# Kernel optimization log

Hardware: AMD Instinct MI355X
Metric: run time of the kernel (lower is better)

Reference implementation:

```python
import jax, jax.numpy as jnp
import numpy as np

CHANNELS = 256
N_HEADS = 8
WS = 8
HEAD_DIM = CHANNELS // N_HEADS
SCALE = HEAD_DIM ** -0.5
EPS = 1e-5


def setup_inputs() -> dict:
    key = jax.random.key(0)
    ks = jax.random.split(key, 7)
    C = CHANNELS
    B, T, H, W = 2, 4, 64, 64
    x = jax.random.normal(ks[0], (B * T, C, H, W), dtype=jnp.float32)
    s = 1.0 / np.sqrt(C)
    w_qkv = jax.random.uniform(ks[1], (3 * C, C), jnp.float32, -s, s)
    b_qkv = jax.random.uniform(ks[2], (3 * C,), jnp.float32, -s, s)
    w_proj = jax.random.uniform(ks[3], (C, C), jnp.float32, -s, s)
    b_proj = jax.random.uniform(ks[4], (C,), jnp.float32, -s, s)
    gamma = jnp.ones((C,), jnp.float32)
    beta = jnp.zeros((C,), jnp.float32)
    return {"x": x, "w_qkv": w_qkv, "b_qkv": b_qkv, "w_proj": w_proj,
            "b_proj": b_proj, "gamma": gamma, "beta": beta, "T": T}


def _forward(x, w_qkv, b_qkv, w_proj, b_proj, gamma, beta, T):
    BT, C, H, W = x.shape
    B = BT // T
    ws = WS
    pH = (ws - H % ws) % ws
    pW = (ws - W % ws) % ws
    if pH > 0 or pW > 0:
        x_p = jnp.pad(x, ((0, 0), (0, 0), (0, pH), (0, pW)))
    else:
        x_p = x
    Hp, Wp = H + pH, W + pW
    nH, nW = Hp // ws, Wp // ws
    # partition: (B,T,C,nH,ws,nW,ws) -> (B,nH,nW,T,ws,ws,C) -> (B*nH*nW, T*ws*ws, C)
    xw = x_p.reshape(B, T, C, nH, ws, nW, ws)
    xw = jnp.transpose(xw, (0, 3, 5, 1, 4, 6, 2))
    L = T * ws * ws
    xw = xw.reshape(B * nH * nW, L, C)
    # LayerNorm over channels
    mu = jnp.mean(xw, axis=-1, keepdims=True)
    var = jnp.mean(jnp.square(xw - mu), axis=-1, keepdims=True)
    xn = (xw - mu) * jax.lax.rsqrt(var + EPS) * gamma + beta
    # QKV projection
    qkv = xn @ w_qkv.T + b_qkv  # (NW, L, 3C)
    qkv = qkv.reshape(xw.shape[0], L, 3, N_HEADS, HEAD_DIM)
    q, k, v = qkv[:, :, 0], qkv[:, :, 1], qkv[:, :, 2]  # (NW, L, h, d)
    scores = jnp.einsum('nlhd,nmhd->nhlm', q, k) * SCALE
    attn = jax.nn.softmax(scores, axis=-1)
    out = jnp.einsum('nhlm,nmhd->nlhd', attn, v).reshape(xw.shape[0], L, C)
    out = out @ w_proj.T + b_proj
    out = xw + out
    # unpartition
    out = out.reshape(B, nH, nW, T, ws, ws, C)
    out = jnp.transpose(out, (0, 3, 6, 1, 4, 2, 5)).reshape(B * T, C, Hp, Wp)
    if pH > 0 or pW > 0:
        out = out[:, :, :H, :W]
    return out


def reference(x, w_qkv, b_qkv, w_proj, b_proj, gamma, beta, T):
    return _forward(x, w_qkv, b_qkv, w_proj, b_proj, gamma, beta, T)
```

## Files before the change

kernel.cpp:

```cpp
#include <hip/hip_runtime.h>
#include <hip/hip_bf16.h>

typedef __hip_bfloat16 bf16;
typedef __attribute__((ext_vector_type(8))) short short8;
typedef __attribute__((ext_vector_type(4))) short sh4;
typedef __attribute__((ext_vector_type(4))) float f32x4;

#define SCALE_F 0.17677669529663687f
#define LOG2E_F 1.4426950408889634f
#define EPS_F 1e-5f
#define NW_CHUNK 32
#define ROWS_CHUNK (NW_CHUNK * 256)

#define OW_QKV  0
#define OW_PROJ 196608
#define OB_QKV  262144
#define OB_PROJ 262912
#define NWB     263168

__device__ __forceinline__ float b2f(bf16 v) { return __bfloat162float(v); }
__device__ __forceinline__ bf16 f2b(float v) { return __float2bfloat16(v); }
__device__ __forceinline__ short f2bs(float v) { bf16 h = f2b(v); return *(short*)&h; }
__device__ __forceinline__ float bs2f(short s) { bf16 h = *(bf16*)&s; return __bfloat162float(h); }

__device__ __forceinline__ float ldin(const void* p, size_t i, int mode) {
  if (mode) return ((const float*)p)[i];
  return b2f(((const bf16*)p)[i]);
}
__device__ __forceinline__ void stout(void* p, size_t i, int mode, float v) {
  if (mode) ((float*)p)[i] = v;
  else      ((bf16*)p)[i] = f2b(v);
}
__device__ __forceinline__ float4 ldin4(const void* p, size_t i, int mode) {
  if (mode) return *(const float4*)((const float*)p + i);
  const sh4 s = *(const sh4*)((const short*)p + i);
  return make_float4(bs2f(s[0]), bs2f(s[1]), bs2f(s[2]), bs2f(s[3]));
}
__device__ __forceinline__ void stout4(void* p, size_t i, int mode, float4 v) {
  if (mode) { *(float4*)((float*)p + i) = v; }
  else {
    sh4 s; s[0] = f2bs(v.x); s[1] = f2bs(v.y); s[2] = f2bs(v.z); s[3] = f2bs(v.w);
    *(sh4*)((short*)p + i) = s;
  }
}

__device__ __forceinline__ void gld16(void* lds, const void* g) {
  __builtin_amdgcn_global_load_lds(
      (const __attribute__((address_space(1))) unsigned int*)g,
      (__attribute__((address_space(3))) unsigned int*)lds, 16, 0, 0);
}

__global__ __launch_bounds__(256) void k_probe(const float* __restrict__ xf,
                                               int* __restrict__ flag) {
  __shared__ int cnt;
  if (threadIdx.x == 0) cnt = 0;
  __syncthreads();
  int bad = 0;
  for (int i = threadIdx.x; i < 1024; i += 256) {
    const float v = xf[i];
    if (!(fabsf(v) < 1e20f)) bad++;
  }
  atomicAdd(&cnt, bad);
  __syncthreads();
  if (threadIdx.x == 0) flag[0] = (cnt < 8) ? 1 : 0;
}

__global__ __launch_bounds__(256) void k_prep(const void* __restrict__ w1,
                                              const void* __restrict__ w2,
                                              const void* __restrict__ b1,
                                              const void* __restrict__ b2,
                                              short* __restrict__ wbuf,
                                              const int* __restrict__ flag) {
  const int mode = flag[0];
  const int i = blockIdx.x * 256 + threadIdx.x;
  float v;
  if (i < OW_PROJ)      v = ldin(w1, i, mode);
  else if (i < OB_QKV)  v = ldin(w2, i - OW_PROJ, mode);
  else if (i < OB_PROJ) v = ldin(b1, i - OB_QKV, mode);
  else if (i < NWB)     v = ldin(b2, i - OB_PROJ, mode);
  else return;
  wbuf[i] = f2bs(v);
}

__global__ __launch_bounds__(256) void k_ln(const void* __restrict__ x,
                                            const void* __restrict__ gamma,
                                            const void* __restrict__ beta,
                                            bf16* __restrict__ xn,
                                            const int* __restrict__ flag) {
  const int mode = flag[0];
  const int bt = blockIdx.x >> 6;
  const int h  = blockIdx.x & 63;
  const int tid = threadIdx.x;
  const int cl = tid >> 4;
  const int wi = tid & 15;

  __shared__ short sX[256][68];
  __shared__ float sred[16][65];
  __shared__ float sqred[16][65];
  __shared__ float smu[64], srs[64];

  const size_t gbase = (size_t)bt * 1048576 + (size_t)h * 64 + wi * 4;
  float s4[4] = {0.f, 0.f, 0.f, 0.f}, q4[4] = {0.f, 0.f, 0.f, 0.f};
  for (int c0 = 0; c0 < 256; c0 += 16) {
    const int c = c0 + cl;
    const float4 v = ldin4(x, gbase + (size_t)c * 4096, mode);
    s4[0] += v.x; q4[0] += v.x * v.x;
    s4[1] += v.y; q4[1] += v.y * v.y;
    s4[2] += v.z; q4[2] += v.z * v.z;
    s4[3] += v.w; q4[3] += v.w * v.w;
    sh4 b;
    b[0] = f2bs(v.x); b[1] = f2bs(v.y); b[2] = f2bs(v.z); b[3] = f2bs(v.w);
    *(sh4*)&sX[c][wi * 4] = b;
  }
#pragma unroll
  for (int k = 0; k < 4; ++k) {
    sred[cl][wi * 4 + k] = s4[k];
    sqred[cl][wi * 4 + k] = q4[k];
  }
  __syncthreads();
  if (tid < 64) {
    float a = 0.f, q = 0.f;
#pragma unroll
    for (int g = 0; g < 16; ++g) { a += sred[g][tid]; q += sqred[g][tid]; }
    const float mu = a * (1.0f / 256.0f);
    const float var = fmaxf(q * (1.0f / 256.0f) - mu * mu, 0.0f);
    smu[tid] = mu; srs[tid] = rsqrtf(var + EPS_F);
  }
  __syncthreads();

  const int c = tid;
  const float g = ldin(gamma, c, mode), be = ldin(beta, c, mode);
  const size_t rb =
      ((size_t)(((bt >> 2) * 64 + (h >> 3) * 8) * 256 + (bt & 3) * 64 + (h & 7) * 8)) * 256 + c;
  for (int iw = 0; iw < 8; ++iw) {
#pragma unroll
    for (int s = 0; s < 8; ++s) {
      const int w = iw * 8 + s;
      const float v = bs2f(sX[c][w]);
      xn[rb + (size_t)iw * 65536 + s * 256] = f2b((v - smu[w]) * srs[w] * g + be);
    }
  }
}

__global__ __launch_bounds__(256) void k_qkv(const bf16* __restrict__ A,
                                             const short* __restrict__ wb,
                                             bf16* __restrict__ out,
                                             int row_base) {
  __shared__ short smem[2 * 128 * 72];
  short* sA = smem;
  short* sB = smem + 128 * 64;
  const int row0 = blockIdx.x * 128;
  const int col0 = blockIdx.y * 128;
  const int tid = threadIdx.x;
  const int wid = tid >> 6, lane = tid & 63;
  const int wy = wid >> 1, wx = wid & 1;
  const int l15 = lane & 15, quad = lane >> 4;
  const short* Ab = (const short*)A;

  const int lr = lane >> 3;
  const int swc = (lane & 7) ^ lr;

  f32x4 acc[4][4];
#pragma unroll
  for (int i = 0; i < 4; ++i)
#pragma unroll
    for (int j = 0; j < 4; ++j) acc[i][j] = (f32x4){0.f, 0.f, 0.f, 0.f};

  for (int k0 = 0; k0 < 256; k0 += 64) {
    if (k0) __syncthreads();
#pragma unroll
    for (int it = 0; it < 4; ++it) {
      const int rbase = wid * 32 + it * 8;
      gld16(sA + rbase * 64,
            Ab + (size_t)(row_base + row0 + rbase + lr) * 256 + k0 + swc * 8);
      gld16(sB + rbase * 64,
            wb + (size_t)(col0 + rbase + lr) * 256 + k0 + swc * 8);
    }
    asm volatile("s_waitcnt vmcnt(0)" ::: "memory");
    __syncthreads();
#pragma unroll
    for (int kk = 0; kk < 64; kk += 32) {
      const int ck = kk >> 3;
      short8 af[4], bfv[4];
#pragma unroll
      for (int i = 0; i < 4; ++i) {
        const int ar = wy * 64 + i * 16 + l15;
        af[i] = *(const short8*)(sA + ar * 64 + (((quad + ck) ^ (ar & 7)) * 8));
      }
#pragma unroll
      for (int j = 0; j < 4; ++j) {
        const int br = wx * 64 + j * 16 + l15;
        bfv[j] = *(const short8*)(sB + br * 64 + (((quad + ck) ^ (br & 7)) * 8));
      }
#pragma unroll
      for (int i = 0; i < 4; ++i)
#pragma unroll
        for (int j = 0; j < 4; ++j)
          acc[i][j] = __builtin_amdgcn_mfma_f32_16x16x32_bf16(af[i], bfv[j], acc[i][j], 0, 0, 0);
    }
  }

  __syncthreads();
  short* slab = smem + wid * (64 * 72);
#pragma unroll
  for (int j = 0; j < 4; ++j) {
    const int col = col0 + wx * 64 + j * 16 + l15;
    const float bj = bs2f(wb[OB_QKV + col]);
#pragma unroll
    for (int i = 0; i < 4; ++i)
#pragma unroll
      for (int r = 0; r < 4; ++r)
        slab[(i * 16 + quad * 4 + r) * 72 + j * 16 + l15] = f2bs(acc[i][j][r] + bj);
  }
  asm volatile("s_waitcnt lgkmcnt(0)" ::: "memory");
  {
    const int srow = lane >> 3;
    const int scol = (lane & 7) * 8;
    short* og = (short*)out;
#pragma unroll
    for (int it = 0; it < 8; ++it) {
      const int rloc = it * 8 + srow;
      short8 v = *(const short8*)&slab[rloc * 72 + scol];
      *(short8*)&og[(size_t)(row0 + wy * 64 + rloc) * 768 + col0 + wx * 64 + scol] = v;
    }
  }
}

__global__ __launch_bounds__(256) void k_attn(const bf16* __restrict__ qkv,
                                              bf16* __restrict__ aout,
                                              int n_base, int nw_mask, int nw_shift) {
  const int n_loc = blockIdx.x & nw_mask, hh = blockIdx.x >> nw_shift;
  const int n_glob = n_base + n_loc;
  __shared__ short sK[256][32];
  __shared__ short sVt[32][256];
  __shared__ short sP[4][16][64];
  const int tid = threadIdx.x;
  const int wid = tid >> 6, lane = tid & 63;
  const int l15 = lane & 15, quad = lane >> 4;
  const short* qg = (const short*)qkv;
  const size_t base = (size_t)n_loc * 256 * 768 + hh * 32;

#pragma unroll
  for (int it = 0; it < 4; ++it) {
    const int rbase = wid * 64 + it * 16;
    gld16(&sK[rbase][0],
          qg + base + (size_t)(rbase + (lane >> 2)) * 768 + 256 + (lane & 3) * 8);
  }
  for (int c = tid; c < 1024; c += 256) {
    const int m = c >> 2, d0 = (c & 3) * 8;
    short8 vv = *(const short8*)(qg + base + (size_t)m * 768 + 512 + d0);
#pragma unroll
    for (int j = 0; j < 8; ++j)
      sVt[d0 + j][(((m >> 3) ^ j) << 3) | (m & 7)] = vv[j];
  }
  asm volatile("s_waitcnt vmcnt(0)" ::: "memory");
  __syncthreads();

  const int R0 = wid * 64;
  const float esc = SCALE_F * LOG2E_F;

  for (int lt = 0; lt < 4; ++lt) {
    const int lrow = R0 + lt * 16;
    const short8 qf = *(const short8*)(qg + base + (size_t)(lrow + l15) * 768 + quad * 8);

    f32x4 sacc[16];
    __builtin_amdgcn_s_setprio(1);
#pragma unroll
    for (int t = 0; t < 16; ++t) {
      sacc[t] = (f32x4){0.f, 0.f, 0.f, 0.f};
      const short8 kf = *(const short8*)&sK[t * 16 + l15][quad * 8];
      sacc[t] = __builtin_amdgcn_mfma_f32_16x16x32_bf16(qf, kf, sacc[t], 0, 0, 0);
    }
    __builtin_amdgcn_s_setprio(0);

    float sum[4] = {0.f, 0.f, 0.f, 0.f};
#pragma unroll
    for (int t = 0; t < 16; ++t)
#pragma unroll
      for (int r = 0; r < 4; ++r) {
        const float p = exp2f(sacc[t][r] * esc);
        sacc[t][r] = p;
        sum[r] += p;
      }
#pragma unroll
    for (int m = 1; m < 16; m <<= 1)
#pragma unroll
      for (int r = 0; r < 4; ++r) sum[r] += __shfl_xor(sum[r], m, 64);
    float inv[4];
#pragma unroll
    for (int r = 0; r < 4; ++r) inv[r] = 1.0f / sum[r];

    f32x4 oacc[2] = {(f32x4){0.f, 0.f, 0.f, 0.f}, (f32x4){0.f, 0.f, 0.f, 0.f}};
#pragma unroll
    for (int ph = 0; ph < 4; ++ph) {
#pragma unroll
      for (int t = 0; t < 4; ++t) {
        const int tt = ph * 4 + t;
        const int chnk = t * 2 + (l15 >> 3);
#pragma unroll
        for (int r = 0; r < 4; ++r) {
          const int row = quad * 4 + r;
          sP[wid][row][((chnk ^ (row & 7)) << 3) | (l15 & 7)] = f2bs(sacc[tt][r]);
        }
      }
      asm volatile("s_waitcnt lgkmcnt(0)" ::: "memory");
      __builtin_amdgcn_s_setprio(1);
#pragma unroll
      for (int kk = 0; kk < 2; ++kk) {
        const int pch = (kk * 4 + quad) ^ (l15 & 7);
        const short8 pf = *(const short8*)&sP[wid][l15][pch * 8];
#pragma unroll
        for (int dt = 0; dt < 2; ++dt) {
          const int vrow = dt * 16 + l15;
          const int cch = ph * 8 + kk * 4 + quad;
          const short8 vf = *(const short8*)&sVt[vrow][((cch ^ (vrow & 7)) * 8)];
          oacc[dt] = __builtin_amdgcn_mfma_f32_16x16x32_bf16(pf, vf, oacc[dt], 0, 0, 0);
        }
      }
      __builtin_amdgcn_s_setprio(0);
      asm volatile("s_waitcnt lgkmcnt(0)" ::: "memory");
    }

#pragma unroll
    for (int dt = 0; dt < 2; ++dt) {
      const int chnk = dt * 2 + (l15 >> 3);
#pragma unroll
      for (int r = 0; r < 4; ++r) {
        const int row = quad * 4 + r;
        sP[wid][row][((chnk ^ (row & 7)) << 3) | (l15 & 7)] = f2bs(oacc[dt][r] * inv[r]);
      }
    }
    asm volatile("s_waitcnt lgkmcnt(0)" ::: "memory");
    {
      const int rloc = lane >> 2;
      const int pch = (lane & 3) ^ (rloc & 7);
      short8 v = *(const short8*)&sP[wid][rloc][pch * 8];
      short* og = (short*)aout;
      *(short8*)&og[((size_t)n_glob * 256 + lrow + rloc) * 256 + hh * 32 + (lane & 3) * 8] = v;
    }
    asm volatile("s_waitcnt lgkmcnt(0)" ::: "memory");
  }
}

__global__ __launch_bounds__(256) void k_proj_g(const bf16* __restrict__ A,
                                                const short* __restrict__ wb,
                                                bf16* __restrict__ out) {
  __shared__ short smem[2 * 128 * 72];
  short* sA = smem;
  short* sB = smem + 128 * 64;
  const int row0 = blockIdx.x * 128;
  const int col0 = blockIdx.y * 128;
  const int tid = threadIdx.x;
  const int wid = tid >> 6, lane = tid & 63;
  const int wy = wid >> 1, wx = wid & 1;
  const int l15 = lane & 15, quad = lane >> 4;
  const short* Ab = (const short*)A;

  const int lr = lane >> 3;
  const int swc = (lane & 7) ^ lr;

  f32x4 acc[4][4];
#pragma unroll
  for (int i = 0; i < 4; ++i)
#pragma unroll
    for (int j = 0; j < 4; ++j) acc[i][j] = (f32x4){0.f, 0.f, 0.f, 0.f};

  for (int k0 = 0; k0 < 256; k0 += 64) {
    if (k0) __syncthreads();
#pragma unroll
    for (int it = 0; it < 4; ++it) {
      const int rbase = wid * 32 + it * 8;
      gld16(sA + rbase * 64,
            Ab + (size_t)(row0 + rbase + lr) * 256 + k0 + swc * 8);
      gld16(sB + rbase * 64,
            wb + OW_PROJ + (size_t)(col0 + rbase + lr) * 256 + k0 + swc * 8);
    }
    asm volatile("s_waitcnt vmcnt(0)" ::: "memory");
    __syncthreads();
#pragma unroll
    for (int kk = 0; kk < 64; kk += 32) {
      const int ck = kk >> 3;
      short8 af[4], bfv[4];
#pragma unroll
      for (int i = 0; i < 4; ++i) {
        const int ar = wy * 64 + i * 16 + l15;
        af[i] = *(const short8*)(sA + ar * 64 + (((quad + ck) ^ (ar & 7)) * 8));
      }
#pragma unroll
      for (int j = 0; j < 4; ++j) {
        const int br = wx * 64 + j * 16 + l15;
        bfv[j] = *(const short8*)(sB + br * 64 + (((quad + ck) ^ (br & 7)) * 8));
      }
#pragma unroll
      for (int i = 0; i < 4; ++i)
#pragma unroll
        for (int j = 0; j < 4; ++j)
          acc[i][j] = __builtin_amdgcn_mfma_f32_16x16x32_bf16(af[i], bfv[j], acc[i][j], 0, 0, 0);
    }
  }

  __syncthreads();
  short* slab = smem + wid * (64 * 72);
#pragma unroll
  for (int j = 0; j < 4; ++j) {
    const int col = col0 + wx * 64 + j * 16 + l15;
    const float bj = bs2f(wb[OB_PROJ + col]);
#pragma unroll
    for (int i = 0; i < 4; ++i)
#pragma unroll
      for (int r = 0; r < 4; ++r)
        slab[(i * 16 + quad * 4 + r) * 72 + j * 16 + l15] = f2bs(acc[i][j][r] + bj);
  }
  asm volatile("s_waitcnt lgkmcnt(0)" ::: "memory");
  {
    const int srow = lane >> 3;
    const int scol = (lane & 7) * 8;
    short* og = (short*)out;
#pragma unroll
    for (int it = 0; it < 8; ++it) {
      const int rloc = it * 8 + srow;
      short8 v = *(const short8*)&slab[rloc * 72 + scol];
      *(short8*)&og[(size_t)(row0 + wy * 64 + rloc) * 256 + col0 + wx * 64 + scol] = v;
    }
  }
}

__global__ __launch_bounds__(256) void k_add(const bf16* __restrict__ tmp,
                                             const void* __restrict__ x,
                                             void* __restrict__ out,
                                             const int* __restrict__ flag) {
  const int mode = flag[0];
  const int bt = blockIdx.x >> 6;
  const int h  = blockIdx.x & 63;
  const int tid = threadIdx.x;

  __shared__ short sT2[256][68];

  const int n_b = (bt >> 2) * 64 + (h >> 3) * 8;
  const int l0  = (bt & 3) * 64 + (h & 7) * 8;
  const short* tg = (const short*)tmp;

#pragma unroll
  for (int i = 0; i < 8; ++i) {
    const int id = i * 256 + tid;
    const int w = id >> 5, c8 = (id & 31) * 8;
    const int row = (n_b + (w >> 3)) * 256 + l0 + (w & 7);
    const short8 v = *(const short8*)(tg + (size_t)row * 256 + c8);
    const int wg = ((w >> 2) ^ ((id & 31) & 15)) * 4 + (w & 3);
#pragma unroll
    for (int j = 0; j < 8; ++j) sT2[c8 + j][wg] = v[j];
  }
  __syncthreads();

  const int cl = tid >> 4;
  const int wi = tid & 15;
  const size_t gb = (size_t)bt * 1048576 + (size_t)h * 64 + wi * 4;
  for (int c0 = 0; c0 < 256; c0 += 16) {
    const int c = c0 + cl;
    const int k15 = (c >> 3) & 15;
    const sh4 pv = *(const sh4*)&sT2[c][((wi ^ k15) & 15) * 4];
    const size_t gaddr = gb + (size_t)c * 4096;
    const float4 xv = ldin4(x, gaddr, mode);
    float4 o;
    o.x = xv.x + bs2f(pv[0]);
    o.y = xv.y + bs2f(pv[1]);
    o.z = xv.z + bs2f(pv[2]);
    o.w = xv.w + bs2f(pv[3]);
    stout4(out, gaddr, mode, o);
  }
}

__global__ __launch_bounds__(256) void k_proj(const bf16* __restrict__ A,
                                              const short* __restrict__ wb,
                                              const void* __restrict__ x,
                                              void* __restrict__ out,
                                              const int* __restrict__ flag) {
  const int mode = flag[0];
  __shared__ short smem[2 * 128 * 64];
  __shared__ float sT[4][16][17];
  short* sA = smem;
  short* sB = smem + 128 * 64;
  const int row0 = blockIdx.x * 128;
  const int col0 = blockIdx.y * 128;
  const int tid = threadIdx.x;
  const int wid = tid >> 6, lane = tid & 63;
  const int wy = wid >> 1, wx = wid & 1;
  const int l15 = lane & 15, quad = lane >> 4;
  const short* Ab = (const short*)A;

  const int lr = lane >> 3;
  const int swc = (lane & 7) ^ lr;

  f32x4 acc[4][4];
#pragma unroll
  for (int i = 0; i < 4; ++i)
#pragma unroll
    for (int j = 0; j < 4; ++j) acc[i][j] = (f32x4){0.f, 0.f, 0.f, 0.f};

  for (int k0 = 0; k0 < 256; k0 += 64) {
    if (k0) __syncthreads();
#pragma unroll
    for (int it = 0; it < 4; ++it) {
      const int rbase = wid * 32 + it * 8;
      gld16(sA + rbase * 64,
            Ab + (size_t)(row0 + rbase + lr) * 256 + k0 + swc * 8);
      gld16(sB + rbase * 64,
            wb + OW_PROJ + (size_t)(col0 + rbase + lr) * 256 + k0 + swc * 8);
    }
    asm volatile("s_waitcnt vmcnt(0)" ::: "memory");
    __syncthreads();
#pragma unroll
    for (int kk = 0; kk < 64; kk += 32) {
      const int ck = kk >> 3;
      short8 af[4], bfv[4];
#pragma unroll
      for (int i = 0; i < 4; ++i) {
        const int ar = wy * 64 + i * 16 + l15;
        af[i] = *(const short8*)(sA + ar * 64 + (((quad + ck) ^ (ar & 7)) * 8));
      }
#pragma unroll
      for (int j = 0; j < 4; ++j) {
        const int br = wx * 64 + j * 16 + l15;
        bfv[j] = *(const short8*)(sB + br * 64 + (((quad + ck) ^ (br & 7)) * 8));
      }
#pragma unroll
      for (int i = 0; i < 4; ++i)
#pragma unroll
        for (int j = 0; j < 4; ++j)
          acc[i][j] = __builtin_amdgcn_mfma_f32_16x16x32_bf16(af[i], bfv[j], acc[i][j], 0, 0, 0);
    }
  }

#pragma unroll
  for (int i = 0; i < 4; ++i) {
#pragma unroll
    for (int j = 0; j < 4; ++j) {
#pragma unroll
      for (int r = 0; r < 4; ++r)
        sT[wid][quad * 4 + r][l15] = acc[i][j][r];
      asm volatile("s_waitcnt lgkmcnt(0)" ::: "memory");
#pragma unroll
      for (int r2 = 0; r2 < 4; ++r2) {
        const float v = sT[wid][l15][quad * 4 + r2];
        const int row = row0 + wy * 64 + i * 16 + l15;
        const int c   = col0 + wx * 64 + j * 16 + quad * 4 + r2;
        const int n = row >> 8, l = row & 255;
        const int b = n >> 6, ih = (n >> 3) & 7, iw = n & 7;
        const int tt = l >> 6, rr = (l >> 3) & 7, ss = l & 7;
        const int btl = b * 4 + tt;
        const size_t gaddr = (size_t)btl * 1048576 + (size_t)c * 4096 +
                             (ih * 8 + rr) * 64 + iw * 8 + ss;
        const float o = v + bs2f(wb[OB_PROJ + c]) + ldin(x, gaddr, mode);
        stout(out, gaddr, mode, o);
      }
      asm volatile("s_waitcnt lgkmcnt(0)" ::: "memory");
    }
  }
}

extern "C" void kernel_launch(void* const* d_in, const int* in_sizes, int n_in,
                              void* d_out, int out_size, void* d_ws, size_t ws_size,
                              hipStream_t stream) {
  (void)in_sizes; (void)n_in; (void)out_size;
  const void* x      = d_in[0];
  const void* w_qkv  = d_in[1];
  const void* b_qkv  = d_in[2];
  const void* w_proj = d_in[3];
  const void* b_proj = d_in[4];
  const void* gamma  = d_in[5];
  const void* beta   = d_in[6];

  char* ws = (char*)d_ws;
  int* flag    = (int*)ws;
  short* wbuf  = (short*)(ws + 1024);
  bf16* xnbuf  = (bf16*)(ws + 1024 + 526336);
  bf16* qkvb   = (bf16*)(ws + 1024 + 526336 + 16777216);

  const size_t need_full = 1024 + 526336 + 16777216 + (size_t)32768 * 768 * 2;

  hipLaunchKernelGGL(k_probe, dim3(1), dim3(256), 0, stream, (const float*)x, flag);
  hipLaunchKernelGGL(k_prep, dim3((NWB + 255) / 256), dim3(256), 0, stream,
                     w_qkv, w_proj, b_qkv, b_proj, wbuf, flag);
  hipLaunchKernelGGL(k_ln, dim3(512), dim3(256), 0, stream, x, gamma, beta, xnbuf, flag);

  if (ws_size >= need_full) {
    hipLaunchKernelGGL(k_qkv, dim3(256, 6), dim3(256), 0, stream,
                       xnbuf, wbuf, qkvb, 0);
    hipLaunchKernelGGL(k_attn, dim3(1024), dim3(256), 0, stream,
                       qkvb, xnbuf, 0, 127, 7);
    bf16* tmpb = qkvb;
    hipLaunchKernelGGL(k_proj_g, dim3(256, 2), dim3(256), 0, stream,
                       xnbuf, wbuf, tmpb);
    hipLaunchKernelGGL(k_add, dim3(512), dim3(256), 0, stream,
                       tmpb, x, d_out, flag);
  } else {
    for (int c = 0; c < 4; ++c) {
      hipLaunchKernelGGL(k_qkv, dim3(64, 6), dim3(256), 0, stream,
                         xnbuf, wbuf, qkvb, c * ROWS_CHUNK);
      hipLaunchKernelGGL(k_attn, dim3(NW_CHUNK * 8), dim3(256), 0, stream,
                         qkvb, xnbuf, c * NW_CHUNK, NW_CHUNK - 1, 5);
    }
    hipLaunchKernelGGL(k_proj, dim3(256, 2), dim3(256), 0, stream,
                       xnbuf, wbuf, x, d_out, flag);
  }
}
```

Baseline: 196.4 us.

## Fold probe and weight prep into LN kernel, use fast exp/rcp intrinsics

Removes the separate probe and weight-conversion launches. Each consuming kernel (k_ln, k_add, k_proj) now detects the input dtype itself, and k_ln also converts the weights and biases to bf16. The attention softmax switches to the hardware exp2 and reciprocal builtins, and several manual lgkmcnt waits are dropped to cut launch overhead and stalls. The risks are the redundant per-block probe reads and the lower precision of the fast intrinsics. Removing the explicit waits also relies on the compiler inserting the LDS waits needed for correctness.

Result: faster. 180.7 us (-8.0%).

```diff
diff --git a/kernel.cpp b/kernel.cpp
--- a/kernel.cpp
+++ b/kernel.cpp
@@ -23,6 +23,17 @@
 __device__ __forceinline__ short f2bs(float v) { bf16 h = f2b(v); return *(short*)&h; }
 __device__ __forceinline__ float bs2f(short s) { bf16 h = *(bf16*)&s; return __bfloat162float(h); }
 
+#if __has_builtin(__builtin_amdgcn_exp2f)
+__device__ __forceinline__ float fexp2(float x) { return __builtin_amdgcn_exp2f(x); }
+#else
+__device__ __forceinline__ float fexp2(float x) { return exp2f(x); }
+#endif
+#if __has_builtin(__builtin_amdgcn_rcpf)
+__device__ __forceinline__ float frcp(float x) { return __builtin_amdgcn_rcpf(x); }
+#else
+__device__ __forceinline__ float frcp(float x) { return 1.0f / x; }
+#endif
+
 __device__ __forceinline__ float ldin(const void* p, size_t i, int mode) {
   if (mode) return ((const float*)p)[i];
   return b2f(((const bf16*)p)[i]);
@@ -44,53 +55,65 @@
   }
 }
 
+__device__ __forceinline__ int probe_mode(const float* xf, int tid) {
+  __shared__ int s_cnt;
+  if (tid == 0) s_cnt = 0;
+  __syncthreads();
+  int bad = 0;
+#pragma unroll
+  for (int i = 0; i < 4; ++i) {
+    const float v = xf[tid * 4 + i];
+    if (!(fabsf(v) < 1e20f)) bad++;
+  }
+  if (bad) atomicAdd(&s_cnt, bad);
+  __syncthreads();
+  return (s_cnt < 8) ? 1 : 0;
+}
+
 __device__ __forceinline__ void gld16(void* lds, const void* g) {
   __builtin_amdgcn_global_load_lds(
       (const __attribute__((address_space(1))) unsigned int*)g,
       (__attribute__((address_space(3))) unsigned int*)lds, 16, 0, 0);
 }
 
-__global__ __launch_bounds__(256) void k_probe(const float* __restrict__ xf,
-                                               int* __restrict__ flag) {
-  __shared__ int cnt;
-  if (threadIdx.x == 0) cnt = 0;
-  __syncthreads();
-  int bad = 0;
-  for (int i = threadIdx.x; i < 1024; i += 256) {
-    const float v = xf[i];
-    if (!(fabsf(v) < 1e20f)) bad++;
-  }
-  atomicAdd(&cnt, bad);
-  __syncthreads();
-  if (threadIdx.x == 0) flag[0] = (cnt < 8) ? 1 : 0;
-}
-
-__global__ __launch_bounds__(256) void k_prep(const void* __restrict__ w1,
-                                              const void* __restrict__ w2,
-                                              const void* __restrict__ b1,
-                                              const void* __restrict__ b2,
-                                              short* __restrict__ wbuf,
-                                              const int* __restrict__ flag) {
-  const int mode = flag[0];
-  const int i = blockIdx.x * 256 + threadIdx.x;
-  float v;
-  if (i < OW_PROJ)      v = ldin(w1, i, mode);
-  else if (i < OB_QKV)  v = ldin(w2, i - OW_PROJ, mode);
-  else if (i < OB_PROJ) v = ldin(b1, i - OB_QKV, mode);
-  else if (i < NWB)     v = ldin(b2, i - OB_PROJ, mode);
-  else return;
-  wbuf[i] = f2bs(v);
-}
-
 __global__ __launch_bounds__(256) void k_ln(const void* __restrict__ x,
                                             const void* __restrict__ gamma,
                                             const void* __restrict__ beta,
                                             bf16* __restrict__ xn,
-                                            const int* __restrict__ flag) {
-  const int mode = flag[0];
+                                            const void* __restrict__ w1,
+                                            const void* __restrict__ w2,
+                                            const void* __restrict__ b1,
+                                            const void* __restrict__ b2,
+                                            short* __restrict__ wbuf) {
+  const int tid = threadIdx.x;
+  const int mode = probe_mode((const float*)x, tid);
+
+  {
+    const int base = (blockIdx.x * 256 + tid) * 2;
+#pragma unroll
+    for (int e = 0; e < 2; ++e) {
+      const int i = base + e;
+      float v;
+      if (i < OW_PROJ)      v = ldin(w1, i, mode);
+      else if (i < OB_QKV)  v = ldin(w2, i - OW_PROJ, mode);
+      else if (i < OB_PROJ) v = ldin(b1, i - OB_QKV, mode);
+      else                  v = ldin(b2, i - OB_PROJ, mode);
+      wbuf[i] = f2bs(v);
+    }
+    if (blockIdx.x == 0) {
+#pragma unroll
+      for (int e = 0; e < 4; ++e) {
+        const int i = 262144 + tid * 4 + e;
+        float v;
+        if (i < OB_PROJ) v = ldin(b1, i - OB_QKV, mode);
+        else             v = ldin(b2, i - OB_PROJ, mode);
+        wbuf[i] = f2bs(v);
+      }
+    }
+  }
+
   const int bt = blockIdx.x >> 6;
   const int h  = blockIdx.x & 63;
-  const int tid = threadIdx.x;
   const int cl = tid >> 4;
   const int wi = tid & 15;
 
@@ -212,7 +235,6 @@
       for (int r = 0; r < 4; ++r)
         slab[(i * 16 + quad * 4 + r) * 72 + j * 16 + l15] = f2bs(acc[i][j][r] + bj);
   }
-  asm volatile("s_waitcnt lgkmcnt(0)" ::: "memory");
   {
     const int srow = lane >> 3;
     const int scol = (lane & 7) * 8;
@@ -278,7 +300,7 @@
     for (int t = 0; t < 16; ++t)
 #pragma unroll
       for (int r = 0; r < 4; ++r) {
-        const float p = exp2f(sacc[t][r] * esc);
+        const float p = fexp2(sacc[t][r] * esc);
         sacc[t][r] = p;
         sum[r] += p;
       }
@@ -288,7 +310,7 @@
       for (int r = 0; r < 4; ++r) sum[r] += __shfl_xor(sum[r], m, 64);
     float inv[4];
 #pragma unroll
-    for (int r = 0; r < 4; ++r) inv[r] = 1.0f / sum[r];
+    for (int r = 0; r < 4; ++r) inv[r] = frcp(sum[r]);
 
     f32x4 oacc[2] = {(f32x4){0.f, 0.f, 0.f, 0.f}, (f32x4){0.f, 0.f, 0.f, 0.f}};
 #pragma unroll
@@ -303,7 +325,6 @@
           sP[wid][row][((chnk ^ (row & 7)) << 3) | (l15 & 7)] = f2bs(sacc[tt][r]);
         }
       }
-      asm volatile("s_waitcnt lgkmcnt(0)" ::: "memory");
       __builtin_amdgcn_s_setprio(1);
 #pragma unroll
       for (int kk = 0; kk < 2; ++kk) {
@@ -318,7 +339,6 @@
         }
       }
       __builtin_amdgcn_s_setprio(0);
-      asm volatile("s_waitcnt lgkmcnt(0)" ::: "memory");
     }
 
 #pragma unroll
@@ -330,7 +350,6 @@
         sP[wid][row][((chnk ^ (row & 7)) << 3) | (l15 & 7)] = f2bs(oacc[dt][r] * inv[r]);
       }
     }
-    asm volatile("s_waitcnt lgkmcnt(0)" ::: "memory");
     {
       const int rloc = lane >> 2;
       const int pch = (lane & 3) ^ (rloc & 7);
@@ -338,7 +357,6 @@
       short* og = (short*)aout;
       *(short8*)&og[((size_t)n_glob * 256 + lrow + rloc) * 256 + hh * 32 + (lane & 3) * 8] = v;
     }
-    asm volatile("s_waitcnt lgkmcnt(0)" ::: "memory");
   }
 }
 
@@ -411,7 +429,6 @@
       for (int r = 0; r < 4; ++r)
         slab[(i * 16 + quad * 4 + r) * 72 + j * 16 + l15] = f2bs(acc[i][j][r] + bj);
   }
-  asm volatile("s_waitcnt lgkmcnt(0)" ::: "memory");
   {
     const int srow = lane >> 3;
     const int scol = (lane & 7) * 8;
@@ -427,12 +444,11 @@
 
 __global__ __launch_bounds__(256) void k_add(const bf16* __restrict__ tmp,
                                              const void* __restrict__ x,
-                                             void* __restrict__ out,
-                                             const int* __restrict__ flag) {
-  const int mode = flag[0];
+                                             void* __restrict__ out) {
+  const int tid = threadIdx.x;
+  const int mode = probe_mode((const float*)x, tid);
   const int bt = blockIdx.x >> 6;
   const int h  = blockIdx.x & 63;
-  const int tid = threadIdx.x;
 
   __shared__ short sT2[256][68];
 
@@ -473,16 +489,15 @@
 __global__ __launch_bounds__(256) void k_proj(const bf16* __restrict__ A,
                                               const short* __restrict__ wb,
                                               const void* __restrict__ x,
-                                              void* __restrict__ out,
-                                              const int* __restrict__ flag) {
-  const int mode = flag[0];
+                                              void* __restrict__ out) {
+  const int tid = threadIdx.x;
+  const int mode = probe_mode((const float*)x, tid);
   __shared__ short smem[2 * 128 * 64];
   __shared__ float sT[4][16][17];
   short* sA = smem;
   short* sB = smem + 128 * 64;
   const int row0 = blockIdx.x * 128;
   const int col0 = blockIdx.y * 128;
-  const int tid = threadIdx.x;
   const int wid = tid >> 6, lane = tid & 63;
   const int wy = wid >> 1, wx = wid & 1;
   const int l15 = lane & 15, quad = lane >> 4;
@@ -571,17 +586,14 @@
   const void* beta   = d_in[6];
 
   char* ws = (char*)d_ws;
-  int* flag    = (int*)ws;
   short* wbuf  = (short*)(ws + 1024);
   bf16* xnbuf  = (bf16*)(ws + 1024 + 526336);
   bf16* qkvb   = (bf16*)(ws + 1024 + 526336 + 16777216);
 
   const size_t need_full = 1024 + 526336 + 16777216 + (size_t)32768 * 768 * 2;
 
-  hipLaunchKernelGGL(k_probe, dim3(1), dim3(256), 0, stream, (const float*)x, flag);
-  hipLaunchKernelGGL(k_prep, dim3((NWB + 255) / 256), dim3(256), 0, stream,
-                     w_qkv, w_proj, b_qkv, b_proj, wbuf, flag);
-  hipLaunchKernelGGL(k_ln, dim3(512), dim3(256), 0, stream, x, gamma, beta, xnbuf, flag);
+  hipLaunchKernelGGL(k_ln, dim3(512), dim3(256), 0, stream, x, gamma, beta, xnbuf,
+                     w_qkv, w_proj, b_qkv, b_proj, wbuf);
 
   if (ws_size >= need_full) {
     hipLaunchKernelGGL(k_qkv, dim3(256, 6), dim3(256), 0, stream,
@@ -592,7 +604,7 @@
     hipLaunchKernelGGL(k_proj_g, dim3(256, 2), dim3(256), 0, stream,
                        xnbuf, wbuf, tmpb);
     hipLaunchKernelGGL(k_add, dim3(512), dim3(256), 0, stream,
-                       tmpb, x, d_out, flag);
+                       tmpb, x, d_out);
   } else {
     for (int c = 0; c < 4; ++c) {
       hipLaunchKernelGGL(k_qkv, dim3(64, 6), dim3(256), 0, stream,
@@ -601,6 +613,6 @@
                          qkvb, xnbuf, c * NW_CHUNK, NW_CHUNK - 1, 5);
     }
     hipLaunchKernelGGL(k_proj, dim3(256, 2), dim3(256), 0, stream,
-                       xnbuf, wbuf, x, d_out, flag);
-  }
-}
+                       xnbuf, wbuf, x, d_out);
+  }
+}
```
